# Optimization experiments

Hardware: AMD Instinct MI355X
Metric: run time of the kernel (lower is better)

Reference implementation:

```python
import jax, jax.numpy as jnp
import numpy as np


def setup_inputs() -> dict:
    key = jax.random.key(0)
    ks = jax.random.split(key, 5)
    B, T, E, C = 4, 1024, 4, 512
    IN, OUT = 2048, 8192
    return {
        "x": jax.random.normal(ks[0], (B, T, IN), dtype=jnp.float32),
        "combine_array": jax.random.uniform(ks[1], (B, T, E, C), dtype=jnp.float32),
        "dispatch_mask": jax.random.uniform(ks[2], (B, T, E, C), dtype=jnp.float32),
        "weight": jax.random.normal(ks[3], (OUT, IN), dtype=jnp.float32) * 0.02,
        "bias": jax.random.normal(ks[4], (OUT,), dtype=jnp.float32) * 0.02,
        "num_experts": E,
    }


def reference(x, combine_array, dispatch_mask, weight, bias, num_experts):
    E = num_experts
    i = weight.shape[1] // E  # expert_in_features
    w = weight.reshape(E, -1, i)  # (E, out, i) -- same reshape as torch
    B = x.shape[0]
    xr = x.reshape(B, -1, E, i)  # (B, T, E, i)
    # dispatch: gather tokens into expert capacity slots via dense mask
    xd = jnp.einsum('btei,btec->beci', xr, dispatch_mask)  # (B, E, C, i)
    # homogeneous coordinates to fold bias into the matmul (as in original)
    x_homo = jnp.concatenate([xd, jnp.ones_like(xd[..., :1])], axis=-1)  # (B,E,C,i+1)
    b_col = jnp.broadcast_to(bias.reshape(1, -1, 1), (E, w.shape[1], 1))
    w_homo = jnp.concatenate([w, b_col], axis=-1)  # (E, out, i+1)
    # per-expert matmul then combine back to tokens
    y = jnp.einsum('beci,eoi->beco', x_homo, w_homo)  # (B, E, C, out)
    return jnp.einsum('beco,btec->bto', y, combine_array)  # (B, T, out)
```

## Files before the change

### kernel.cpp

```cpp
#include <hip/hip_runtime.h>

#define B_   4
#define T_   1024
#define E_   4
#define C_   512
#define IN_  2048
#define OUT_ 8192
#define EI_  512

typedef float f32x4 __attribute__((ext_vector_type(4)));
typedef __bf16 bf16x8 __attribute__((ext_vector_type(8)));
typedef unsigned short ushort8 __attribute__((ext_vector_type(8)));

__device__ __forceinline__ unsigned short f32_bf16(float f) {
  unsigned int u = __float_as_uint(f);
  u += 0x7FFFu + ((u >> 16) & 1u);
  return (unsigned short)(u >> 16);
}

__device__ __forceinline__ void gl2lds16(const void* g, void* l) {
  __builtin_amdgcn_global_load_lds(
      (const __attribute__((address_space(1))) void*)g,
      (__attribute__((address_space(3))) void*)l, 16, 0, 0);
}

#define DSR(dst, addr) do { f32x4 _t_; \
    asm volatile("ds_read_b128 %0, %1" : "=v"(_t_) : "v"(addr)); \
    dst = __builtin_bit_cast(bf16x8, _t_); } while (0)

__global__ __launch_bounds__(256)
void prep(const float* __restrict__ xsrc, const float* __restrict__ msrc,
          const float* __restrict__ combine, const float* __restrict__ weight,
          unsigned short* __restrict__ xdst, unsigned short* __restrict__ mdst,
          unsigned short* __restrict__ comb_bf, float* __restrict__ S,
          unsigned short* __restrict__ W2) {
  const int bid = blockIdx.x;
  const int u = threadIdx.x;
  if (bid < 4096) {
    __shared__ float tile[64][65];
    const int z = bid >> 9;
    const int which = z >> 2;
    const int b = z & 3;
    const int rem = bid & 511;
    const int t0 = (rem >> 5) * 64;
    const int k0 = (rem & 31) * 64;
    const float* src = which ? msrc : xsrc;
    unsigned short* dst = which ? mdst : xdst;
    const int lrow = u >> 4;
    const int lcol = (u & 15) * 4;
    const float* s = src + (size_t)b * (T_ * 2048) + (size_t)t0 * 2048 + k0;
#pragma unroll
    for (int r = 0; r < 4; r++) {
      float4 v = *(const float4*)(s + (size_t)(lrow + 16 * r) * 2048 + lcol);
      tile[lrow + 16 * r][lcol]     = v.x;
      tile[lrow + 16 * r][lcol + 1] = v.y;
      tile[lrow + 16 * r][lcol + 2] = v.z;
      tile[lrow + 16 * r][lcol + 3] = v.w;
    }
    __syncthreads();
    const int kr = u >> 2;
    const int tq = (u & 3) * 8;
    const int kg = k0 + kr;
    const int e  = kg >> 9;
    const int kl = kg & 511;
    unsigned short* d = dst + (((size_t)b * 4 + e) * 512 + kl) * 1024 + t0 + tq;
#pragma unroll
    for (int s8 = 0; s8 < 2; s8++) {
      ushort8 rr;
#pragma unroll
      for (int j = 0; j < 8; j++) rr[j] = f32_bf16(tile[tq + s8 * 32 + j][kr]);
      *(ushort8*)(d + s8 * 32) = rr;
    }
  } else if (bid < 8192) {
    __shared__ float red[256];
    const int row = bid - 4096;
    const float4* p = (const float4*)(combine + (size_t)row * 2048) + (size_t)u * 2;
    float4 a = p[0], b = p[1];
    ushort8 r;
    r[0] = f32_bf16(a.x); r[1] = f32_bf16(a.y);
    r[2] = f32_bf16(a.z); r[3] = f32_bf16(a.w);
    r[4] = f32_bf16(b.x); r[5] = f32_bf16(b.y);
    r[6] = f32_bf16(b.z); r[7] = f32_bf16(b.w);
    *((ushort8*)(comb_bf + (size_t)row * 2048) + u) = r;
    float s = (a.x + a.y + a.z + a.w) + (b.x + b.y + b.z + b.w);
    red[u] = s;
    __syncthreads();
#pragma unroll
    for (int st = 128; st > 0; st >>= 1) {
      if (u < st) red[u] += red[u + st];
      __syncthreads();
    }
    if (u == 0) S[row] = red[0];
  } else {
    const int tid = (bid - 8192) * 256 + u;
    const int i8 = tid & 63;
    const int e  = (tid >> 6) & 3;
    const int o  = tid >> 8;
    const float* s = weight + (size_t)e * 4194304 + (size_t)o * 512 + i8 * 8;
    float4 a = *(const float4*)s;
    float4 b = *(const float4*)(s + 4);
    ushort8 r;
    r[0] = f32_bf16(a.x); r[1] = f32_bf16(a.y);
    r[2] = f32_bf16(a.z); r[3] = f32_bf16(a.w);
    r[4] = f32_bf16(b.x); r[5] = f32_bf16(b.y);
    r[6] = f32_bf16(b.z); r[7] = f32_bf16(b.w);
    *(ushort8*)(W2 + (size_t)o * 2048 + e * 512 + i8 * 8) = r;
  }
}

template <int MODE>
__global__ __launch_bounds__(512, 2)
void gemm_bt(const unsigned short* __restrict__ A,
             const unsigned short* __restrict__ Bm,
             void* __restrict__ Out, const float* __restrict__ bias,
             const float* __restrict__ S,
             int lda, int ldb, int ldo, int K, int Ediv,
             long sAb, long sAe, long sBb, long sBe, long sOb, long sOe) {
  __shared__ __align__(16) char ldsRaw[49152];
  char* ldsg = ldsRaw;
  const unsigned ldsb =
      (unsigned)(unsigned long long)(__attribute__((address_space(3))) char*)(void*)ldsRaw;

  const int u = threadIdx.x;
  const int z = blockIdx.z;
  const int zb = z / Ediv, ze = z % Ediv;
  const unsigned short* Ab = A  + zb * sAb + ze * sAe + (long)(blockIdx.y * 128) * lda;
  const unsigned short* Bb = Bm + zb * sBb + ze * sBe + (long)(blockIdx.x * 128) * ldb;

  const unsigned short* gA = Ab + (long)(u >> 2) * lda + (u & 3) * 8;
  const unsigned short* gB = Bb + (long)(u >> 2) * ldb + (u & 3) * 8;

  const int w = u >> 6, lane = u & 63;
  const int wm = (w & 1) * 64, wn = (w >> 1) * 32;
  const int fm = lane & 15, fk = (lane >> 4) * 8;
  const unsigned aF = (unsigned)((wm + fm) * 64 + fk * 2);
  const unsigned bF = 24576u + (unsigned)((wn + fm) * 64 + fk * 2);
  const unsigned u16 = (unsigned)(u * 16);

  f32x4 acc[4][2] = {};

  const int nt = K / 32;
#define STGBT(buf, kk) do { \
    gl2lds16(gA + (kk) * 32, ldsg + (buf) * 8192 + u16); \
    gl2lds16(gB + (kk) * 32, ldsg + 24576 + (buf) * 8192 + u16); } while (0)

  STGBT(0, 0);
  STGBT(1, 1);
  asm volatile("s_waitcnt vmcnt(2)" ::: "memory");
  __builtin_amdgcn_s_barrier();

  int cur = 0, pre = 2;
  for (int t = 0; t < nt; ++t) {
    bf16x8 af[4], bfv[2];
    const unsigned cb = (unsigned)(cur * 8192);
#pragma unroll
    for (int i = 0; i < 4; i++) DSR(af[i], ldsb + cb + aF + (unsigned)(i * 1024));
#pragma unroll
    for (int j = 0; j < 2; j++) DSR(bfv[j], ldsb + cb + bF + (unsigned)(j * 1024));
    const int kk = (t + 2 < nt) ? t + 2 : nt - 1;
    STGBT(pre, kk);
    asm volatile("s_waitcnt lgkmcnt(0)" ::: "memory");
    __builtin_amdgcn_sched_barrier(0);
    __builtin_amdgcn_s_setprio(1);
#pragma unroll
    for (int i = 0; i < 4; i++)
#pragma unroll
      for (int j = 0; j < 2; j++)
        acc[i][j] = __builtin_amdgcn_mfma_f32_16x16x32_bf16(af[i], bfv[j],
                                                            acc[i][j], 0, 0, 0);
    __builtin_amdgcn_s_setprio(0);
    asm volatile("s_waitcnt vmcnt(2)" ::: "memory");
    __builtin_amdgcn_sched_barrier(0);
    __builtin_amdgcn_s_barrier();
    cur = (cur == 2) ? 0 : cur + 1;
    pre = (pre == 2) ? 0 : pre + 1;
  }
#undef STGBT
  asm volatile("s_waitcnt vmcnt(0)" ::: "memory");

  const long ob = zb * sOb + ze * sOe;
  const int em0 = blockIdx.y * 128 + wm + ((lane >> 4) << 2);
  const int en0 = blockIdx.x * 128 + wn + fm;
  float bcol[2];
  if (MODE == 1) {
#pragma unroll
    for (int j = 0; j < 2; j++) bcol[j] = bias[en0 + j * 16];
  }
#pragma unroll
  for (int i = 0; i < 4; i++)
#pragma unroll
    for (int r = 0; r < 4; r++) {
      const int m = em0 + i * 16 + r;
      const float sm = (MODE == 1) ? S[m] : 0.0f;
#pragma unroll
      for (int j = 0; j < 2; j++) {
        const long off = ob + (long)m * ldo + en0 + j * 16;
        if (MODE == 1)
          ((float*)Out)[off] = acc[i][j][r] + sm * bcol[j];
        else
          ((unsigned short*)Out)[off] = f32_bf16(acc[i][j][r]);
      }
    }
}

__global__ __launch_bounds__(512, 2)
void gemm256(const unsigned short* __restrict__ A,
             const unsigned short* __restrict__ Bm,
             float* __restrict__ Out,
             const float* __restrict__ bias,
             const float* __restrict__ S) {
  __shared__ __align__(16) unsigned short lds[65536];
  char* ldsg = (char*)lds;
  const unsigned ldsb =
      (unsigned)(unsigned long long)(__attribute__((address_space(3))) char*)(void*)lds;

  const int bid = blockIdx.x;
  const int bx = (bid & 7) * 4 + ((bid >> 3) & 3);
  const int by = bid >> 5;

  const int u = threadIdx.x;
  const int w = u >> 6, lane = u & 63;
  const unsigned w1024 = (unsigned)(w * 1024);
  const int wmw = (w >> 2) * 128;
  const int wnw = (w & 3) * 64;
  const int fm = lane & 15;

  const unsigned hi16  = (unsigned)(((lane >> 4) & 3) * 16);
  const unsigned xorv  = (unsigned)((fm & 7) << 4);
  const unsigned colS0 = hi16 ^ xorv;
  const unsigned aR0 = (unsigned)((wmw + fm) * 128) + colS0;
  const unsigned aR1 = aR0 ^ 64u;
  const unsigned bR0 = 65536u + (unsigned)((wnw + fm) * 128) + colS0;
  const unsigned bR1 = bR0 ^ 64u;

  const int srr = w * 8 + (lane >> 3);
  const unsigned swzS = (unsigned)((((lane & 7) ^ ((lane >> 3) & 7)) << 4));
  const char* gA = (const char*)(A  + (size_t)(by * 256) * 2048) + (size_t)srr * 4096 + swzS;
  const char* gB = (const char*)(Bm + (size_t)(bx * 256) * 2048) + (size_t)srr * 4096 + swzS;

#define STG(gsrc, loff) do { \
    gl2lds16((gsrc), ldsg + (loff)); \
    gl2lds16((gsrc) + 262144, ldsg + (loff) + 8192); } while (0)

  STG(gA,                    0u + w1024);
  STG(gA + 524288,       16384u + w1024);
  STG(gB,                65536u + w1024);
  STG(gB + 524288,       81920u + w1024);
  STG(gA + 128,          32768u + w1024);
  STG(gA + 128 + 524288, 49152u + w1024);
  asm volatile("s_waitcnt vmcnt(4)" ::: "memory");
  __builtin_amdgcn_s_barrier();

  f32x4 acc[8][4] = {};
  bf16x8 a0[4][2], a1[4][2], bq[2][2];

  for (int kt = 0; kt < 32; ++kt) {
    const unsigned bbO = (unsigned)((kt & 1) * 32768);
    const unsigned nbR = bbO ^ 32768u;
    const int ktB = (kt + 1 < 32) ? kt + 1 : 31;
    const int ktA = (kt + 2 < 32) ? kt + 2 : 31;
    const char* gBn = gB + ktB * 128;
    const char* gAn = gA + ktA * 128;

#pragma unroll
    for (int i = 0; i < 4; ++i) {
      DSR(a0[i][0], ldsb + bbO + aR0 + (unsigned)(i * 2048));
      DSR(a0[i][1], ldsb + bbO + aR1 + (unsigned)(i * 2048));
    }
#pragma unroll
    for (int j = 0; j < 2; ++j) {
      DSR(bq[j][0], ldsb + bbO + bR0 + (unsigned)(j * 2048));
      DSR(bq[j][1], ldsb + bbO + bR1 + (unsigned)(j * 2048));
    }
    STG(gBn, 65536u + nbR + w1024);
    __builtin_amdgcn_s_barrier();
    asm volatile("s_waitcnt lgkmcnt(0)" ::: "memory");
    __builtin_amdgcn_sched_barrier(0);
    __builtin_amdgcn_s_setprio(1);
#pragma unroll
    for (int i = 0; i < 4; ++i)
#pragma unroll
      for (int j = 0; j < 2; ++j) {
        acc[i][j] = __builtin_amdgcn_mfma_f32_16x16x32_bf16(a0[i][0], bq[j][0], acc[i][j], 0, 0, 0);
        acc[i][j] = __builtin_amdgcn_mfma_f32_16x16x32_bf16(a0[i][1], bq[j][1], acc[i][j], 0, 0, 0);
      }
    __builtin_amdgcn_s_setprio(0);
    __builtin_amdgcn_s_barrier();

#pragma unroll
    for (int i = 0; i < 4; ++i) {
      DSR(a1[i][0], ldsb + bbO + aR0 + (unsigned)((4 + i) * 2048));
      DSR(a1[i][1], ldsb + bbO + aR1 + (unsigned)((4 + i) * 2048));
    }
    STG(gBn + 524288, 81920u + nbR + w1024);
    __builtin_amdgcn_s_barrier();
    asm volatile("s_waitcnt lgkmcnt(0)" ::: "memory");
    __builtin_amdgcn_sched_barrier(0);
    __builtin_amdgcn_s_setprio(1);
#pragma unroll
    for (int i = 0; i < 4; ++i)
#pragma unroll
      for (int j = 0; j < 2; ++j) {
        acc[4 + i][j] = __builtin_amdgcn_mfma_f32_16x16x32_bf16(a1[i][0], bq[j][0], acc[4 + i][j], 0, 0, 0);
        acc[4 + i][j] = __builtin_amdgcn_mfma_f32_16x16x32_bf16(a1[i][1], bq[j][1], acc[4 + i][j], 0, 0, 0);
      }
    __builtin_amdgcn_s_setprio(0);
    __builtin_amdgcn_s_barrier();

#pragma unroll
    for (int j = 0; j < 2; ++j) {
      DSR(bq[j][0], ldsb + bbO + bR0 + (unsigned)((2 + j) * 2048));
      DSR(bq[j][1], ldsb + bbO + bR1 + (unsigned)((2 + j) * 2048));
    }
    STG(gAn, bbO + w1024);
    __builtin_amdgcn_s_barrier();
    asm volatile("s_waitcnt lgkmcnt(0)" ::: "memory");
    __builtin_amdgcn_sched_barrier(0);
    __builtin_amdgcn_s_setprio(1);
#pragma unroll
    for (int i = 0; i < 4; ++i)
#pragma unroll
      for (int j = 0; j < 2; ++j) {
        acc[i][2 + j] = __builtin_amdgcn_mfma_f32_16x16x32_bf16(a0[i][0], bq[j][0], acc[i][2 + j], 0, 0, 0);
        acc[i][2 + j] = __builtin_amdgcn_mfma_f32_16x16x32_bf16(a0[i][1], bq[j][1], acc[i][2 + j], 0, 0, 0);
      }
    __builtin_amdgcn_s_setprio(0);
    __builtin_amdgcn_s_barrier();

    STG(gAn + 524288, bbO + 16384u + w1024);
    __builtin_amdgcn_s_barrier();
    __builtin_amdgcn_s_setprio(1);
#pragma unroll
    for (int i = 0; i < 4; ++i)
#pragma unroll
      for (int j = 0; j < 2; ++j) {
        acc[4 + i][2 + j] = __builtin_amdgcn_mfma_f32_16x16x32_bf16(a1[i][0], bq[j][0], acc[4 + i][2 + j], 0, 0, 0);
        acc[4 + i][2 + j] = __builtin_amdgcn_mfma_f32_16x16x32_bf16(a1[i][1], bq[j][1], acc[4 + i][2 + j], 0, 0, 0);
      }
    __builtin_amdgcn_s_setprio(0);
    asm volatile("s_waitcnt vmcnt(4)" ::: "memory");
    __builtin_amdgcn_sched_barrier(0);
    __builtin_amdgcn_s_barrier();
  }
#undef STG
  asm volatile("s_waitcnt vmcnt(0)" ::: "memory");

  const int m0 = by * 256 + wmw + ((lane >> 4) << 2);
  const int n0 = bx * 256 + wnw + (lane & 15);
  float bc[4];
#pragma unroll
  for (int j = 0; j < 4; ++j) bc[j] = bias[n0 + j * 16];
#pragma unroll
  for (int i = 0; i < 8; ++i)
#pragma unroll
    for (int r = 0; r < 4; ++r) {
      const int m = m0 + i * 16 + r;
      const float sm = S[m];
#pragma unroll
      for (int j = 0; j < 4; ++j)
        Out[(size_t)m * 8192 + n0 + j * 16] = acc[i][j][r] + sm * bc[j];
    }
}

extern "C" void kernel_launch(void* const* d_in, const int* in_sizes, int n_in,
                              void* d_out, int out_size, void* d_ws,
                              size_t ws_size, hipStream_t stream) {
  (void)in_sizes; (void)n_in; (void)out_size; (void)ws_size;
  const float* x       = (const float*)d_in[0];
  const float* combine = (const float*)d_in[1];
  const float* mask    = (const float*)d_in[2];
  const float* weight  = (const float*)d_in[3];
  const float* bias    = (const float*)d_in[4];
  float* out = (float*)d_out;

  char* ws = (char*)d_ws;
  unsigned short* W2      = (unsigned short*)ws;
  unsigned short* comb_bf = (unsigned short*)(ws + 33554432);
  float*          S       = (float*)(ws + 50331648);
  unsigned short* xT      = (unsigned short*)(ws + 51380224);
  unsigned short* maskT   = (unsigned short*)(ws + 68157440);
  unsigned short* xdT     = (unsigned short*)(ws + 84934656);
  unsigned short* zbuf    = (unsigned short*)(ws + 93323264);

  prep<<<16384, 256, 0, stream>>>(x, mask, combine, weight, xT, maskT,
                                  comb_bf, S, W2);

  gemm_bt<0><<<dim3(4, 4, 16), 512, 0, stream>>>(
      xT, maskT, (void*)xdT, nullptr, nullptr, 1024, 1024, 512, 1024,
      4, 2097152L, 524288L, 2097152L, 524288L, 1048576L, 262144L);

  gemm_bt<0><<<dim3(4, 8, 16), 512, 0, stream>>>(
      comb_bf, xdT, (void*)zbuf, nullptr, nullptr, 2048, 512, 2048, 512,
      4, 2097152L, 512L, 1048576L, 262144L, 2097152L, 512L);

  gemm256<<<dim3(512), 512, 0, stream>>>(zbuf, W2, out, bias, S);
}
```

Measured before the change: 402.5 us.

## Load B operand directly into registers and triple-buffer A tiles in LDS

The main GEMM kernel stops staging the B (weight) tile through LDS. Each wave now loads its B fragments straight from global memory into registers, double-buffered across even and odd k-steps. A tiles are staged through a three-slot LDS ring with fewer barriers per step. This cuts LDS traffic and footprint and simplifies synchronisation, but B fragments get no reuse across the waves that share them, and global load latency is exposed more directly.

```diff
diff --git a/kernel.cpp b/kernel.cpp
--- a/kernel.cpp
+++ b/kernel.cpp
@@ -209,10 +209,8 @@
              float* __restrict__ Out,
              const float* __restrict__ bias,
              const float* __restrict__ S) {
-  __shared__ __align__(16) unsigned short lds[65536];
+  __shared__ __align__(16) unsigned short lds[49152];
   char* ldsg = (char*)lds;
-  const unsigned ldsb =
-      (unsigned)(unsigned long long)(__attribute__((address_space(3))) char*)(void*)lds;
 
   const int bid = blockIdx.x;
   const int bx = (bid & 7) * 4 + ((bid >> 3) & 3);
@@ -225,124 +223,92 @@
   const int wnw = (w & 3) * 64;
   const int fm = lane & 15;
 
-  const unsigned hi16  = (unsigned)(((lane >> 4) & 3) * 16);
+  const unsigned hi16  = (unsigned)((lane >> 4) * 16);
   const unsigned xorv  = (unsigned)((fm & 7) << 4);
-  const unsigned colS0 = hi16 ^ xorv;
-  const unsigned aR0 = (unsigned)((wmw + fm) * 128) + colS0;
+  const unsigned aR0 = (unsigned)((wmw + fm) * 128) + (hi16 ^ xorv);
   const unsigned aR1 = aR0 ^ 64u;
-  const unsigned bR0 = 65536u + (unsigned)((wnw + fm) * 128) + colS0;
-  const unsigned bR1 = bR0 ^ 64u;
 
   const int srr = w * 8 + (lane >> 3);
   const unsigned swzS = (unsigned)((((lane & 7) ^ ((lane >> 3) & 7)) << 4));
-  const char* gA = (const char*)(A  + (size_t)(by * 256) * 2048) + (size_t)srr * 4096 + swzS;
-  const char* gB = (const char*)(Bm + (size_t)(bx * 256) * 2048) + (size_t)srr * 4096 + swzS;
-
-#define STG(gsrc, loff) do { \
-    gl2lds16((gsrc), ldsg + (loff)); \
-    gl2lds16((gsrc) + 262144, ldsg + (loff) + 8192); } while (0)
-
-  STG(gA,                    0u + w1024);
-  STG(gA + 524288,       16384u + w1024);
-  STG(gB,                65536u + w1024);
-  STG(gB + 524288,       81920u + w1024);
-  STG(gA + 128,          32768u + w1024);
-  STG(gA + 128 + 524288, 49152u + w1024);
-  asm volatile("s_waitcnt vmcnt(4)" ::: "memory");
+  const char* gA = (const char*)(A + (size_t)(by * 256) * 2048)
+                   + (size_t)srr * 4096 + swzS;
+
+  const char* pB0 = (const char*)Bm + (size_t)(bx * 256 + wnw +  0 + fm) * 4096 + hi16;
+  const char* pB1 = (const char*)Bm + (size_t)(bx * 256 + wnw + 16 + fm) * 4096 + hi16;
+  const char* pB2 = (const char*)Bm + (size_t)(bx * 256 + wnw + 32 + fm) * 4096 + hi16;
+  const char* pB3 = (const char*)Bm + (size_t)(bx * 256 + wnw + 48 + fm) * 4096 + hi16;
+
+#define STGA(kk, loff) do { const char* _s = gA + (kk) * 128; \
+    gl2lds16(_s,          ldsg + (loff) + w1024); \
+    gl2lds16(_s + 262144, ldsg + (loff) + 8192  + w1024); \
+    gl2lds16(_s + 524288, ldsg + (loff) + 16384 + w1024); \
+    gl2lds16(_s + 786432, ldsg + (loff) + 24576 + w1024); } while (0)
+
+#define LOADB(BQ, ko) do { \
+    BQ[0][0] = *(const bf16x8*)(pB0 + (ko)); BQ[0][1] = *(const bf16x8*)(pB0 + (ko) + 64); \
+    BQ[1][0] = *(const bf16x8*)(pB1 + (ko)); BQ[1][1] = *(const bf16x8*)(pB1 + (ko) + 64); \
+    BQ[2][0] = *(const bf16x8*)(pB2 + (ko)); BQ[2][1] = *(const bf16x8*)(pB2 + (ko) + 64); \
+    BQ[3][0] = *(const bf16x8*)(pB3 + (ko)); BQ[3][1] = *(const bf16x8*)(pB3 + (ko) + 64); } while (0)
+
+#define SUBPH(bufS, mh, kh, BQ) do { \
+    bf16x8 av_[4]; \
+    _Pragma("unroll") \
+    for (int i = 0; i < 4; ++i) \
+      av_[i] = *(const bf16x8*)&lds[((bufS) + ((kh) ? aR1 : aR0) \
+                                     + (unsigned)(((mh) * 4 + i) * 2048)) >> 1]; \
+    __builtin_amdgcn_s_setprio(1); \
+    _Pragma("unroll") \
+    for (int i = 0; i < 4; ++i) { \
+      _Pragma("unroll") \
+      for (int j = 0; j < 4; ++j) \
+        acc[(mh) * 4 + i][j] = __builtin_amdgcn_mfma_f32_16x16x32_bf16( \
+            av_[i], BQ[j][kh], acc[(mh) * 4 + i][j], 0, 0, 0); \
+    } \
+    __builtin_amdgcn_s_setprio(0); \
+  } while (0)
+
+  bf16x8 bqE[4][2], bqO[4][2];
+  f32x4 acc[8][4] = {};
+
+  STGA(0, 0u);
+  STGA(1, 32768u);
+  LOADB(bqE, 0);
+  asm volatile("s_waitcnt vmcnt(0)" ::: "memory");
   __builtin_amdgcn_s_barrier();
 
-  f32x4 acc[8][4] = {};
-  bf16x8 a0[4][2], a1[4][2], bq[2][2];
-
-  for (int kt = 0; kt < 32; ++kt) {
-    const unsigned bbO = (unsigned)((kt & 1) * 32768);
-    const unsigned nbR = bbO ^ 32768u;
-    const int ktB = (kt + 1 < 32) ? kt + 1 : 31;
-    const int ktA = (kt + 2 < 32) ? kt + 2 : 31;
-    const char* gBn = gB + ktB * 128;
-    const char* gAn = gA + ktA * 128;
-
-#pragma unroll
-    for (int i = 0; i < 4; ++i) {
-      DSR(a0[i][0], ldsb + bbO + aR0 + (unsigned)(i * 2048));
-      DSR(a0[i][1], ldsb + bbO + aR1 + (unsigned)(i * 2048));
-    }
-#pragma unroll
-    for (int j = 0; j < 2; ++j) {
-      DSR(bq[j][0], ldsb + bbO + bR0 + (unsigned)(j * 2048));
-      DSR(bq[j][1], ldsb + bbO + bR1 + (unsigned)(j * 2048));
-    }
-    STG(gBn, 65536u + nbR + w1024);
+  int c0 = 0;
+  for (int t = 0; t < 16; ++t) {
+    const int c1 = (c0 + 1 == 3) ? 0 : c0 + 1;
+    const int c2 = (c1 + 1 == 3) ? 0 : c1 + 1;
+    const unsigned bufE = (unsigned)(c0 * 32768);
+    const unsigned bufO = (unsigned)(c1 * 32768);
+    const int kE = (2 * t + 2 < 32) ? 2 * t + 2 : 31;
+    const int kO = (2 * t + 3 < 32) ? 2 * t + 3 : 31;
+
+    LOADB(bqO, 128);
+    asm volatile("s_waitcnt vmcnt(12)" ::: "memory");
     __builtin_amdgcn_s_barrier();
-    asm volatile("s_waitcnt lgkmcnt(0)" ::: "memory");
-    __builtin_amdgcn_sched_barrier(0);
-    __builtin_amdgcn_s_setprio(1);
-#pragma unroll
-    for (int i = 0; i < 4; ++i)
-#pragma unroll
-      for (int j = 0; j < 2; ++j) {
-        acc[i][j] = __builtin_amdgcn_mfma_f32_16x16x32_bf16(a0[i][0], bq[j][0], acc[i][j], 0, 0, 0);
-        acc[i][j] = __builtin_amdgcn_mfma_f32_16x16x32_bf16(a0[i][1], bq[j][1], acc[i][j], 0, 0, 0);
-      }
-    __builtin_amdgcn_s_setprio(0);
+    STGA(kE, (unsigned)(c2 * 32768));
+    SUBPH(bufE, 0, 0, bqE);
+    SUBPH(bufE, 0, 1, bqE);
+    SUBPH(bufE, 1, 0, bqE);
+    SUBPH(bufE, 1, 1, bqE);
+
+    LOADB(bqE, 256);
+    asm volatile("s_waitcnt vmcnt(12)" ::: "memory");
     __builtin_amdgcn_s_barrier();
-
-#pragma unroll
-    for (int i = 0; i < 4; ++i) {
-      DSR(a1[i][0], ldsb + bbO + aR0 + (unsigned)((4 + i) * 2048));
-      DSR(a1[i][1], ldsb + bbO + aR1 + (unsigned)((4 + i) * 2048));
-    }
-    STG(gBn + 524288, 81920u + nbR + w1024);
-    __builtin_amdgcn_s_barrier();
-    asm volatile("s_waitcnt lgkmcnt(0)" ::: "memory");
-    __builtin_amdgcn_sched_barrier(0);
-    __builtin_amdgcn_s_setprio(1);
-#pragma unroll
-    for (int i = 0; i < 4; ++i)
-#pragma unroll
-      for (int j = 0; j < 2; ++j) {
-        acc[4 + i][j] = __builtin_amdgcn_mfma_f32_16x16x32_bf16(a1[i][0], bq[j][0], acc[4 + i][j], 0, 0, 0);
-        acc[4 + i][j] = __builtin_amdgcn_mfma_f32_16x16x32_bf16(a1[i][1], bq[j][1], acc[4 + i][j], 0, 0, 0);
-      }
-    __builtin_amdgcn_s_setprio(0);
-    __builtin_amdgcn_s_barrier();
-
-#pragma unroll
-    for (int j = 0; j < 2; ++j) {
-      DSR(bq[j][0], ldsb + bbO + bR0 + (unsigned)((2 + j) * 2048));
-      DSR(bq[j][1], ldsb + bbO + bR1 + (unsigned)((2 + j) * 2048));
-    }
-    STG(gAn, bbO + w1024);
-    __builtin_amdgcn_s_barrier();
-    asm volatile("s_waitcnt lgkmcnt(0)" ::: "memory");
-    __builtin_amdgcn_sched_barrier(0);
-    __builtin_amdgcn_s_setprio(1);
-#pragma unroll
-    for (int i = 0; i < 4; ++i)
-#pragma unroll
-      for (int j = 0; j < 2; ++j) {
-        acc[i][2 + j] = __builtin_amdgcn_mfma_f32_16x16x32_bf16(a0[i][0], bq[j][0], acc[i][2 + j], 0, 0, 0);
-        acc[i][2 + j] = __builtin_amdgcn_mfma_f32_16x16x32_bf16(a0[i][1], bq[j][1], acc[i][2 + j], 0, 0, 0);
-      }
-    __builtin_amdgcn_s_setprio(0);
-    __builtin_amdgcn_s_barrier();
-
-    STG(gAn + 524288, bbO + 16384u + w1024);
-    __builtin_amdgcn_s_barrier();
-    __builtin_amdgcn_s_setprio(1);
-#pragma unroll
-    for (int i = 0; i < 4; ++i)
-#pragma unroll
-      for (int j = 0; j < 2; ++j) {
-        acc[4 + i][2 + j] = __builtin_amdgcn_mfma_f32_16x16x32_bf16(a1[i][0], bq[j][0], acc[4 + i][2 + j], 0, 0, 0);
-        acc[4 + i][2 + j] = __builtin_amdgcn_mfma_f32_16x16x32_bf16(a1[i][1], bq[j][1], acc[4 + i][2 + j], 0, 0, 0);
-      }
-    __builtin_amdgcn_s_setprio(0);
-    asm volatile("s_waitcnt vmcnt(4)" ::: "memory");
-    __builtin_amdgcn_sched_barrier(0);
-    __builtin_amdgcn_s_barrier();
+    STGA(kO, (unsigned)(c0 * 32768));
+    SUBPH(bufO, 0, 0, bqO);
+    SUBPH(bufO, 0, 1, bqO);
+    SUBPH(bufO, 1, 0, bqO);
+    SUBPH(bufO, 1, 1, bqO);
+
+    c0 = c2;
+    pB0 += 256; pB1 += 256; pB2 += 256; pB3 += 256;
   }
-#undef STG
+#undef SUBPH
+#undef LOADB
+#undef STGA
   asm volatile("s_waitcnt vmcnt(0)" ::: "memory");
 
   const int m0 = by * 256 + wmw + ((lane >> 4) << 2);
```

Result: slower. 462.7 us (+15.0%).
